# Kernel tuning notes

Hardware: AMD Instinct MI355X
Metric: run time of the kernel (lower is better)

## Reference

```python
import collections
import functools
import itertools
import math
import jax
import jax.numpy as jnp
import numpy as np

# Weight space: RNN-like {W_ih:(784,512), W_hh:(512,512), b:(512,)}, channels last.
N0, N1, C_IN, C_OUT = 784, 512, 16, 16
PERM_SPEC = [[0, 1], [1, 1], [1]]  # perm-group label per dim of each leaf
N_TERMS = [11, 25, 9]  # equivariant basis terms per output leaf (Bell-number products)


def diagonal_slice(X, matching_dims):
    out = jnp.diagonal(X, axis1=matching_dims[0], axis2=matching_dims[1])
    for dim in matching_dims[2:]:
        out = jnp.diagonal(out, axis1=dim, axis2=-1)
    return out


def find_missing_indices(lstA, lstB):
    setB = set(lstB)
    return [i for i, el in enumerate(lstA) if el not in setB]


def get_repeated_idcs(lst):
    index_map = {}
    for index, item in enumerate(lst):
        index_map.setdefault(item, []).append(index)
    return [idcs for idcs in index_map.values() if len(idcs) > 1]


def match_dim_order(X, X_idcs, out_idcs):
    X_idcs_copy = X_idcs[:]
    perm = []
    for idx in out_idcs:
        if idx in X_idcs_copy:
            i = X_idcs_copy.index(idx)
            perm.append(i)
            X_idcs_copy[i] = None
    X = jnp.transpose(X, perm)
    return X, [X_idcs[i] for i in perm]


def remove_idcs(lst, idcs):
    return [l for i, l in enumerate(lst) if i not in idcs]


def move_dims_to_end(X, dims):
    new_in_order = remove_idcs(list(range(X.ndim)), dims) + dims
    return jnp.transpose(X, new_in_order)


def generate_partitions(items):
    if len(items) == 1:
        yield [items]
        return
    first = items[0]
    for subpart in generate_partitions(items[1:]):
        for n, subset in enumerate(subpart):
            yield subpart[:n] + [[first] + subset] + subpart[n + 1:]
        yield [[first]] + subpart


def valid_partitions(indices, perms):
    groups = collections.defaultdict(list)
    for index, perm in zip(indices, perms):
        groups[perm].append(index)
    parts_per_group = [list(generate_partitions(g)) for g in groups.values()]
    for p in itertools.product(*parts_per_group):
        yield [s for s in itertools.chain(*p)]


def gen_terms(out_spec, in_spec, out_shape, inp):
    """Basis terms of an equivariant linear map from in_spec to out_spec."""
    terms = []
    k1, k2 = len(out_spec), len(in_spec)
    for partition in valid_partitions(list(range(k1 + k2)), list(out_spec) + list(in_spec)):
        indices = [-1] * (k1 + k2)
        for subset_idx, subset in enumerate(partition):
            for dim in subset:
                indices[dim] = subset_idx
        out_indices, in_indices = indices[:k1], indices[k1:]
        term = inp
        # Collapse repeated input indices via diagonals.
        while (rep_idcs := get_repeated_idcs(in_indices)):
            term = diagonal_slice(term, rep_idcs[0])
            idx = in_indices[rep_idcs[0][0]]
            in_indices = remove_idcs(in_indices, rep_idcs[0])
            in_indices.append(idx)
        # Mean-reduce input dims that do not appear in the output.
        agg_idcs = find_missing_indices(in_indices, out_indices)
        term = jnp.mean(term, axis=agg_idcs)
        in_indices = remove_idcs(in_indices, agg_idcs)
        # Scatter onto diagonals for repeated output indices.
        for diag_set in get_repeated_idcs(out_indices):
            dim_size, out_idx = out_shape[diag_set[0]], out_indices[diag_set[0]]
            matching_in_dims = [i for i, idx in enumerate(in_indices) if idx == out_idx]
            num_new_dims = len(diag_set) - len(matching_in_dims)
            term = move_dims_to_end(term, matching_in_dims)
            new_term = jnp.zeros(term.shape + (dim_size,) * num_new_dims, dtype=term.dtype)
            diag_slice = (jnp.s_[:],) * (new_term.ndim - len(diag_set)) + (jnp.arange(dim_size),) * len(diag_set)
            if not matching_in_dims:
                term = jnp.expand_dims(term, axis=-1)
            term = new_term.at[diag_slice].add(term)
            in_indices = remove_idcs(in_indices, matching_in_dims)
            in_indices.extend([out_idx] * len(diag_set))
        term, in_indices = match_dim_order(term, in_indices, out_indices)
        term = jnp.expand_dims(term, axis=find_missing_indices(out_indices, in_indices))
        terms.append(term)
    return terms


def setup_inputs() -> dict:
    key = jax.random.key(0)
    ks = jax.random.split(key, 6)
    inp = {
        "w_ih": jax.random.normal(ks[0], (N0, N1, C_IN), jnp.float32),
        "w_hh": jax.random.normal(ks[1], (N1, N1, C_IN), jnp.float32),
        "b": jax.random.normal(ks[2], (N1, C_IN), jnp.float32),
    }
    for i, n in enumerate(N_TERMS):
        scale = math.sqrt(2.0 / (C_IN * n))  # 'he' init, fan_in = c_in * n_terms
        inp[f"theta_{i}"] = scale * jax.random.normal(ks[3 + i], (n, C_IN, C_OUT), jnp.float32)
        inp[f"bias_{i}"] = jnp.zeros((C_OUT,), jnp.float32)
    return inp


def reference(w_ih, w_hh, b, theta_0, theta_1, theta_2, bias_0, bias_1, bias_2):
    flat_params = [w_ih, w_hh, b]
    thetas = [theta_0, theta_1, theta_2]
    biases = [bias_0, bias_1, bias_2]
    outs = []
    for i in range(3):
        terms_i = []
        for j in range(3):
            gen = jax.vmap(
                functools.partial(gen_terms, PERM_SPEC[i], PERM_SPEC[j], flat_params[i].shape),
                in_axes=-1, out_axes=-1)
            terms_i.extend(gen(flat_params[j]))
        out = biases[i]
        for k, term in enumerate(terms_i):
            out = out + term @ thetas[i][k]  # [..., c_in] @ [c_in, c_out]
        outs.append(out)
    return tuple(outs)
```

## Files before the change

### kernel.cpp

```cpp
#include <hip/hip_runtime.h>


#define N0 784
#define N1 512

__global__ __launch_bounds__(256)
void k_stage1(const float* __restrict__ wih, const float* __restrict__ whh,
              float* __restrict__ rm_ih, float* __restrict__ cm_ih,
              float* __restrict__ rm_hh, float* __restrict__ cm_hh,
              float* __restrict__ d_hh) {
  __shared__ float4 red[256];
  int t = threadIdx.x;
  if (blockIdx.x < N0) {
    int a = blockIdx.x;
    const float4* row = (const float4*)(wih + (size_t)a * 8192);
    float4 acc = make_float4(0.f, 0.f, 0.f, 0.f);
    for (int j = t; j < 2048; j += 256) {
      float4 v = row[j];
      acc.x += v.x; acc.y += v.y; acc.z += v.z; acc.w += v.w;
    }
    red[t] = acc; __syncthreads();
    #pragma unroll
    for (int s = 128; s >= 4; s >>= 1) {
      if (t < s) {
        float4 o = red[t + s], m = red[t];
        m.x += o.x; m.y += o.y; m.z += o.z; m.w += o.w;
        red[t] = m;
      }
      __syncthreads();
    }
    if (t < 4) {
      float4 m = red[t];
      const float s = 1.0f / 512.0f;
      float4 o = make_float4(m.x * s, m.y * s, m.z * s, m.w * s);
      ((float4*)(rm_ih + a * 16))[t] = o;
    }
    return;
  }
  int b = blockIdx.x - N0;
  int q = t & 3, g = t >> 2;

  float4 acc = make_float4(0.f, 0.f, 0.f, 0.f);
  for (int a = g; a < N0; a += 64) {
    float4 v = *(const float4*)(wih + (size_t)a * 8192 + b * 16 + q * 4);
    acc.x += v.x; acc.y += v.y; acc.z += v.z; acc.w += v.w;
  }
  red[t] = acc; __syncthreads();
  #pragma unroll
  for (int s = 128; s >= 4; s >>= 1) {
    if (t < s) {
      float4 o = red[t + s], m = red[t];
      m.x += o.x; m.y += o.y; m.z += o.z; m.w += o.w;
      red[t] = m;
    }
    __syncthreads();
  }
  if (t < 4) {
    float4 m = red[t];
    const float s = 1.0f / 784.0f;
    ((float4*)(cm_ih + b * 16))[t] = make_float4(m.x * s, m.y * s, m.z * s, m.w * s);
  }
  __syncthreads();

  const float4* rowp = (const float4*)(whh + (size_t)b * 8192);
  acc = make_float4(0.f, 0.f, 0.f, 0.f);
  for (int n = t; n < 2048; n += 256) {
    float4 v = rowp[n];
    acc.x += v.x; acc.y += v.y; acc.z += v.z; acc.w += v.w;
  }
  red[t] = acc; __syncthreads();
  #pragma unroll
  for (int s = 128; s >= 4; s >>= 1) {
    if (t < s) {
      float4 o = red[t + s], m = red[t];
      m.x += o.x; m.y += o.y; m.z += o.z; m.w += o.w;
      red[t] = m;
    }
    __syncthreads();
  }
  if (t < 4) {
    float4 m = red[t];
    const float s = 1.0f / 512.0f;
    ((float4*)(rm_hh + b * 16))[t] = make_float4(m.x * s, m.y * s, m.z * s, m.w * s);
  }
  __syncthreads();

  acc = make_float4(0.f, 0.f, 0.f, 0.f);
  for (int a = g; a < N1; a += 64) {
    float4 v = *(const float4*)(whh + (size_t)a * 8192 + b * 16 + q * 4);
    acc.x += v.x; acc.y += v.y; acc.z += v.z; acc.w += v.w;
  }
  red[t] = acc; __syncthreads();
  #pragma unroll
  for (int s = 128; s >= 4; s >>= 1) {
    if (t < s) {
      float4 o = red[t + s], m = red[t];
      m.x += o.x; m.y += o.y; m.z += o.z; m.w += o.w;
      red[t] = m;
    }
    __syncthreads();
  }
  if (t < 4) {
    float4 m = red[t];
    const float s = 1.0f / 512.0f;
    ((float4*)(cm_hh + b * 16))[t] = make_float4(m.x * s, m.y * s, m.z * s, m.w * s);
    ((float4*)(d_hh + b * 16))[t] = *(const float4*)(whh + (size_t)b * 8192 + b * 16 + t * 4);
  }
}

__global__ __launch_bounds__(256)
void k_vec(const float* __restrict__ rm_ih, const float* __restrict__ cm_ih,
           const float* __restrict__ rm_hh, const float* __restrict__ cm_hh,
           const float* __restrict__ d_hh, const float* __restrict__ bvec,
           const float* __restrict__ th0, const float* __restrict__ bias0,
           const float* __restrict__ th1, const float* __restrict__ bias1,
           const float* __restrict__ th2, const float* __restrict__ bias2,
           float* __restrict__ A0C, float* __restrict__ B0,
           float* __restrict__ A1C, float* __restrict__ B1,
           float* __restrict__ DD1, float* __restrict__ out2) {
  __shared__ float redf[256];
  __shared__ float4 red4[256];
  __shared__ float gv[4][16];
  __shared__ float sc[64];
  int t = threadIdx.x, ci = t & 15, g = t >> 4;

  {
    float acc = 0.f;
    for (int a = g; a < N0; a += 16) acc += rm_ih[a * 16 + ci];
    redf[t] = acc; __syncthreads();
    for (int s = 128; s >= 16; s >>= 1) { if (t < s) redf[t] += redf[t + s]; __syncthreads(); }
    if (t < 16) gv[0][t] = redf[t] * (1.0f / 784.0f);
    __syncthreads();
    acc = 0.f;
    for (int a = g; a < N1; a += 16) acc += d_hh[a * 16 + ci];
    redf[t] = acc; __syncthreads();
    for (int s = 128; s >= 16; s >>= 1) { if (t < s) redf[t] += redf[t + s]; __syncthreads(); }
    if (t < 16) gv[1][t] = redf[t] * (1.0f / 512.0f);
    __syncthreads();
    acc = 0.f;
    for (int a = g; a < N1; a += 16) acc += rm_hh[a * 16 + ci];
    redf[t] = acc; __syncthreads();
    for (int s = 128; s >= 16; s >>= 1) { if (t < s) redf[t] += redf[t + s]; __syncthreads(); }
    if (t < 16) gv[2][t] = redf[t] * (1.0f / 512.0f);
    __syncthreads();
    acc = 0.f;
    for (int a = g; a < N1; a += 16) acc += bvec[a * 16 + ci];
    redf[t] = acc; __syncthreads();
    for (int s = 128; s >= 16; s >>= 1) { if (t < s) redf[t] += redf[t + s]; __syncthreads(); }
    if (t < 16) gv[3][t] = redf[t] * (1.0f / 512.0f);
    __syncthreads();
  }
  {
    int co = ci, j = g, o = j * 16 + co;
    float g0 = gv[0][j], dm = gv[1][j], gh = gv[2][j], mv = gv[3][j];
    float4 p;
    p.x = g0 * th0[768 + o]  + dm * th0[1280 + o] + gh * th0[2048 + o] + mv * th0[2560 + o];
    p.y = g0 * th1[1024 + o] + dm * th1[2304 + o] + gh * th1[4864 + o] + mv * th1[6144 + o];
    p.z = g0 * th1[512 + o]  + dm * th1[1792 + o] + gh * th1[4096 + o] + mv * th1[5632 + o];
    p.w = g0 * th2[256 + o]  + dm * th2[768 + o]  + gh * th2[1536 + o] + mv * th2[2048 + o];
    red4[t] = p; __syncthreads();
    for (int s = 128; s >= 16; s >>= 1) {
      if (t < s) {
        float4 a = red4[t], b = red4[t + s];
        a.x += b.x; a.y += b.y; a.z += b.z; a.w += b.w;
        red4[t] = a;
      }
      __syncthreads();
    }
    if (t < 16) {
      float4 a = red4[t];
      sc[t] = a.x + bias0[t];
      sc[16 + t] = a.y + bias1[t];
      sc[32 + t] = a.z + bias2[t] * 0.f + 0.f;
      sc[32 + t] = a.z;
      sc[48 + t] = a.w + bias2[t];
    }
    __syncthreads();
  }
  int idx = blockIdx.x * 256 + t;
  int i = idx >> 4, co = idx & 15;
  if (i >= N0) return;
  float a0 = sc[co];
  for (int k = 0; k < 16; k++) a0 += rm_ih[i * 16 + k] * th0[256 + k * 16 + co];
  A0C[idx] = a0;
  if (i < N1) {
    float b0a = 0.f, a1 = sc[16 + co], b1a = 0.f, dd = sc[32 + co], o2 = sc[48 + co];
    for (int k = 0; k < 16; k++) {
      float cmi = cm_ih[i * 16 + k], d = d_hh[i * 16 + k], r = rm_hh[i * 16 + k];
      float cm = cm_hh[i * 16 + k], v = bvec[i * 16 + k];
      int o = k * 16 + co;
      b0a += cmi * th0[512 + o]  + d * th0[1024 + o] + r * th0[1536 + o] + cm * th0[1792 + o] + v * th0[2304 + o];
      a1  += cmi * th1[768 + o]  + d * th1[2048 + o] + r * th1[4352 + o] + cm * th1[4608 + o] + v * th1[5888 + o];
      b1a += cmi * th1[256 + o]  + d * th1[1536 + o] + r * th1[3072 + o] + cm * th1[3840 + o] + v * th1[5376 + o];
      dd  += cmi * th1[0 + o]    + d * th1[1280 + o] + r * th1[2560 + o] + cm * th1[3584 + o] + v * th1[5120 + o];
      o2  += cmi * th2[0 + o]    + d * th2[512 + o]  + r * th2[1024 + o] + cm * th2[1280 + o] + v * th2[1792 + o];
    }
    B0[idx] = b0a; A1C[idx] = a1; B1[idx] = b1a; DD1[idx] = dd; out2[idx] = o2;
  }
}

__global__ __launch_bounds__(256)
void k_out(const float* __restrict__ wih, const float* __restrict__ whh,
           const float* __restrict__ th0, const float* __restrict__ th1,
           const float* __restrict__ A0C, const float* __restrict__ B0,
           const float* __restrict__ A1C, const float* __restrict__ B1,
           const float* __restrict__ DD1,
           float* __restrict__ out0, float* __restrict__ out1) {
  if (blockIdx.x < 1024) {
    int tid = blockIdx.x * 256 + threadIdx.x;
    int q = tid & 3;
    int slot = tid >> 2;
    const int nslots = (1024 * 256) >> 2;
    float4 tq[16];
    #pragma unroll
    for (int k = 0; k < 16; k++) tq[k] = *(const float4*)(th0 + k * 16 + q * 4);
    for (int p = slot; p < N0 * N1; p += nslots) {
      const float4* row = (const float4*)(wih + (size_t)p * 16);
      float4 r0 = row[0], r1 = row[1], r2 = row[2], r3 = row[3];
      int a = p >> 9, bb = p & 511;
      float4 acc = *(const float4*)(A0C + a * 16 + q * 4);
      float4 b4 = *(const float4*)(B0 + bb * 16 + q * 4);
      acc.x += b4.x; acc.y += b4.y; acc.z += b4.z; acc.w += b4.w;
      float wv[16] = { r0.x, r0.y, r0.z, r0.w, r1.x, r1.y, r1.z, r1.w,
                       r2.x, r2.y, r2.z, r2.w, r3.x, r3.y, r3.z, r3.w };
      #pragma unroll
      for (int k = 0; k < 16; k++) {
        acc.x += wv[k] * tq[k].x; acc.y += wv[k] * tq[k].y;
        acc.z += wv[k] * tq[k].z; acc.w += wv[k] * tq[k].w;
      }
      *(float4*)(out0 + (size_t)p * 16 + q * 4) = acc;
    }
  } else {
    int tid = (blockIdx.x - 1024) * 256 + threadIdx.x;
    int q = tid & 7;
    int slot = tid >> 3;
    const int nslots = (1024 * 256) >> 3;
    float2 tA[16], tB[16];
    #pragma unroll
    for (int k = 0; k < 16; k++) {
      tA[k] = *(const float2*)(th1 + 13 * 256 + k * 16 + q * 2);
      tB[k] = *(const float2*)(th1 + 11 * 256 + k * 16 + q * 2);
    }
    for (int p = slot; p < N1 * N1; p += nslots) {
      int a = p >> 9, b = p & 511;
      const float4* ra = (const float4*)(whh + (size_t)p * 16);
      const float4* rt = (const float4*)(whh + (size_t)((b << 9) | a) * 16);
      float4 a0 = ra[0], a1v = ra[1], a2 = ra[2], a3 = ra[3];
      float4 t0 = rt[0], t1v = rt[1], t2 = rt[2], t3 = rt[3];
      float2 acc = *(const float2*)(A1C + a * 16 + q * 2);
      float2 bb = *(const float2*)(B1 + b * 16 + q * 2);
      acc.x += bb.x; acc.y += bb.y;
      if (a == b) {
        float2 dd = *(const float2*)(DD1 + a * 16 + q * 2);
        acc.x += dd.x; acc.y += dd.y;
      }
      float ya[16] = { a0.x, a0.y, a0.z, a0.w, a1v.x, a1v.y, a1v.z, a1v.w,
                       a2.x, a2.y, a2.z, a2.w, a3.x, a3.y, a3.z, a3.w };
      float yt[16] = { t0.x, t0.y, t0.z, t0.w, t1v.x, t1v.y, t1v.z, t1v.w,
                       t2.x, t2.y, t2.z, t2.w, t3.x, t3.y, t3.z, t3.w };
      #pragma unroll
      for (int k = 0; k < 16; k++) {
        acc.x += ya[k] * tA[k].x + yt[k] * tB[k].x;
        acc.y += ya[k] * tA[k].y + yt[k] * tB[k].y;
      }
      *(float2*)(out1 + (size_t)p * 16 + q * 2) = acc;
    }
  }
}

extern "C" void kernel_launch(void* const* d_in, const int* in_sizes, int n_in,
                              void* d_out, int out_size, void* d_ws, size_t ws_size,
                              hipStream_t stream) {
  const float* w_ih = (const float*)d_in[0];
  const float* w_hh = (const float*)d_in[1];
  const float* bvec = (const float*)d_in[2];
  const float *th0, *bias0, *th1, *bias1, *th2, *bias2;
  if (n_in >= 9 && in_sizes[4] == 16) {
    th0 = (const float*)d_in[3]; bias0 = (const float*)d_in[4];
    th1 = (const float*)d_in[5]; bias1 = (const float*)d_in[6];
    th2 = (const float*)d_in[7]; bias2 = (const float*)d_in[8];
  } else {
    th0 = (const float*)d_in[3]; th1 = (const float*)d_in[4]; th2 = (const float*)d_in[5];
    bias0 = (const float*)d_in[6]; bias1 = (const float*)d_in[7]; bias2 = (const float*)d_in[8];
  }
  float* ws    = (float*)d_ws;
  float* rm_ih = ws;
  float* cm_ih = rm_ih + 12544;
  float* rm_hh = cm_ih + 8192;
  float* cm_hh = rm_hh + 8192;
  float* d_hh  = cm_hh + 8192;
  float* A0C   = d_hh + 8192;
  float* B0    = A0C + 12544;
  float* A1C   = B0 + 8192;
  float* B1    = A1C + 8192;
  float* DD1   = B1 + 8192;
  float* out0 = (float*)d_out;
  float* out1 = out0 + (size_t)N0 * N1 * 16;
  float* out2 = out1 + (size_t)N1 * N1 * 16;

  hipLaunchKernelGGL(k_stage1, dim3(N0 + N1), dim3(256), 0, stream,
                     w_ih, w_hh, rm_ih, cm_ih, rm_hh, cm_hh, d_hh);
  hipLaunchKernelGGL(k_vec, dim3(49), dim3(256), 0, stream,
                     rm_ih, cm_ih, rm_hh, cm_hh, d_hh, bvec,
                     th0, bias0, th1, bias1, th2, bias2,
                     A0C, B0, A1C, B1, DD1, out2);
  hipLaunchKernelGGL(k_out, dim3(2048), dim3(256), 0, stream,
                     w_ih, w_hh, th0, th1, A0C, B0, A1C, B1, DD1, out0, out1);
}
```

Baseline: 177.4 us.

## Split stage1 reductions into separate blocks and stage theta in LDS in k_vec

Stage1 now launches one block per reduction (row and column means for both matrices) instead of having each hh block run three reductions one after another. This spreads the serial work across more blocks to raise parallelism. k_vec copies all theta tensors into shared memory, reduces the global vectors with float4 accesses, and uses vectorized per-row loads. The cost is about 46KB of LDS per block and an extra copy of theta in every block. The `i >= N0` guard was removed; this is safe only because 49 blocks exactly covers 784x16 elements.

```diff
diff --git a/kernel.cpp b/kernel.cpp
--- a/kernel.cpp
+++ b/kernel.cpp
@@ -3,6 +3,10 @@
 
 #define N0 784
 #define N1 512
+
+__device__ __forceinline__ float4 f4add(float4 a, float4 b) {
+  a.x += b.x; a.y += b.y; a.z += b.z; a.w += b.w; return a;
+}
 
 __global__ __launch_bounds__(256)
 void k_stage1(const float* __restrict__ wih, const float* __restrict__ whh,
@@ -10,101 +14,40 @@
               float* __restrict__ rm_hh, float* __restrict__ cm_hh,
               float* __restrict__ d_hh) {
   __shared__ float4 red[256];
-  int t = threadIdx.x;
-  if (blockIdx.x < N0) {
-    int a = blockIdx.x;
-    const float4* row = (const float4*)(wih + (size_t)a * 8192);
-    float4 acc = make_float4(0.f, 0.f, 0.f, 0.f);
-    for (int j = t; j < 2048; j += 256) {
-      float4 v = row[j];
-      acc.x += v.x; acc.y += v.y; acc.z += v.z; acc.w += v.w;
-    }
-    red[t] = acc; __syncthreads();
-    #pragma unroll
-    for (int s = 128; s >= 4; s >>= 1) {
-      if (t < s) {
-        float4 o = red[t + s], m = red[t];
-        m.x += o.x; m.y += o.y; m.z += o.z; m.w += o.w;
-        red[t] = m;
-      }
-      __syncthreads();
-    }
-    if (t < 4) {
-      float4 m = red[t];
-      const float s = 1.0f / 512.0f;
-      float4 o = make_float4(m.x * s, m.y * s, m.z * s, m.w * s);
-      ((float4*)(rm_ih + a * 16))[t] = o;
-    }
-    return;
-  }
-  int b = blockIdx.x - N0;
-  int q = t & 3, g = t >> 2;
-
+  int t = threadIdx.x, blk = blockIdx.x;
   float4 acc = make_float4(0.f, 0.f, 0.f, 0.f);
-  for (int a = g; a < N0; a += 64) {
-    float4 v = *(const float4*)(wih + (size_t)a * 8192 + b * 16 + q * 4);
-    acc.x += v.x; acc.y += v.y; acc.z += v.z; acc.w += v.w;
+  float scale;
+  float* dst;
+  if (blk < N0) {
+    const float4* row = (const float4*)(wih + (size_t)blk * 8192);
+    for (int j = t; j < 2048; j += 256) acc = f4add(acc, row[j]);
+    scale = 1.f / 512.f; dst = rm_ih + blk * 16;
+  } else if (blk < N0 + N1) {
+    int b = blk - N0, q = t & 3, g = t >> 2;
+    for (int a = g; a < N0; a += 64)
+      acc = f4add(acc, *(const float4*)(wih + (size_t)a * 8192 + b * 16 + q * 4));
+    scale = 1.f / 784.f; dst = cm_ih + b * 16;
+  } else if (blk < N0 + 2 * N1) {
+    int b = blk - N0 - N1;
+    const float4* row = (const float4*)(whh + (size_t)b * 8192);
+    for (int j = t; j < 2048; j += 256) acc = f4add(acc, row[j]);
+    scale = 1.f / 512.f; dst = rm_hh + b * 16;
+  } else {
+    int b = blk - N0 - 2 * N1, q = t & 3, g = t >> 2;
+    for (int a = g; a < N1; a += 64)
+      acc = f4add(acc, *(const float4*)(whh + (size_t)a * 8192 + b * 16 + q * 4));
+    scale = 1.f / 512.f; dst = cm_hh + b * 16;
+    if (t < 4) ((float4*)(d_hh + b * 16))[t] = *(const float4*)(whh + (size_t)b * 8192 + b * 16 + t * 4);
   }
   red[t] = acc; __syncthreads();
   #pragma unroll
   for (int s = 128; s >= 4; s >>= 1) {
-    if (t < s) {
-      float4 o = red[t + s], m = red[t];
-      m.x += o.x; m.y += o.y; m.z += o.z; m.w += o.w;
-      red[t] = m;
-    }
+    if (t < s) red[t] = f4add(red[t], red[t + s]);
     __syncthreads();
   }
   if (t < 4) {
     float4 m = red[t];
-    const float s = 1.0f / 784.0f;
-    ((float4*)(cm_ih + b * 16))[t] = make_float4(m.x * s, m.y * s, m.z * s, m.w * s);
-  }
-  __syncthreads();
-
-  const float4* rowp = (const float4*)(whh + (size_t)b * 8192);
-  acc = make_float4(0.f, 0.f, 0.f, 0.f);
-  for (int n = t; n < 2048; n += 256) {
-    float4 v = rowp[n];
-    acc.x += v.x; acc.y += v.y; acc.z += v.z; acc.w += v.w;
-  }
-  red[t] = acc; __syncthreads();
-  #pragma unroll
-  for (int s = 128; s >= 4; s >>= 1) {
-    if (t < s) {
-      float4 o = red[t + s], m = red[t];
-      m.x += o.x; m.y += o.y; m.z += o.z; m.w += o.w;
-      red[t] = m;
-    }
-    __syncthreads();
-  }
-  if (t < 4) {
-    float4 m = red[t];
-    const float s = 1.0f / 512.0f;
-    ((float4*)(rm_hh + b * 16))[t] = make_float4(m.x * s, m.y * s, m.z * s, m.w * s);
-  }
-  __syncthreads();
-
-  acc = make_float4(0.f, 0.f, 0.f, 0.f);
-  for (int a = g; a < N1; a += 64) {
-    float4 v = *(const float4*)(whh + (size_t)a * 8192 + b * 16 + q * 4);
-    acc.x += v.x; acc.y += v.y; acc.z += v.z; acc.w += v.w;
-  }
-  red[t] = acc; __syncthreads();
-  #pragma unroll
-  for (int s = 128; s >= 4; s >>= 1) {
-    if (t < s) {
-      float4 o = red[t + s], m = red[t];
-      m.x += o.x; m.y += o.y; m.z += o.z; m.w += o.w;
-      red[t] = m;
-    }
-    __syncthreads();
-  }
-  if (t < 4) {
-    float4 m = red[t];
-    const float s = 1.0f / 512.0f;
-    ((float4*)(cm_hh + b * 16))[t] = make_float4(m.x * s, m.y * s, m.z * s, m.w * s);
-    ((float4*)(d_hh + b * 16))[t] = *(const float4*)(whh + (size_t)b * 8192 + b * 16 + t * 4);
+    ((float4*)dst)[t] = make_float4(m.x * scale, m.y * scale, m.z * scale, m.w * scale);
   }
 }
 
@@ -118,60 +61,64 @@
            float* __restrict__ A0C, float* __restrict__ B0,
            float* __restrict__ A1C, float* __restrict__ B1,
            float* __restrict__ DD1, float* __restrict__ out2) {
-  __shared__ float redf[256];
-  __shared__ float4 red4[256];
+  __shared__ float th[11520];
+  __shared__ float4 red[256];
   __shared__ float gv[4][16];
   __shared__ float sc[64];
-  int t = threadIdx.x, ci = t & 15, g = t >> 4;
-
-  {
-    float acc = 0.f;
-    for (int a = g; a < N0; a += 16) acc += rm_ih[a * 16 + ci];
-    redf[t] = acc; __syncthreads();
-    for (int s = 128; s >= 16; s >>= 1) { if (t < s) redf[t] += redf[t + s]; __syncthreads(); }
-    if (t < 16) gv[0][t] = redf[t] * (1.0f / 784.0f);
-    __syncthreads();
-    acc = 0.f;
-    for (int a = g; a < N1; a += 16) acc += d_hh[a * 16 + ci];
-    redf[t] = acc; __syncthreads();
-    for (int s = 128; s >= 16; s >>= 1) { if (t < s) redf[t] += redf[t + s]; __syncthreads(); }
-    if (t < 16) gv[1][t] = redf[t] * (1.0f / 512.0f);
-    __syncthreads();
-    acc = 0.f;
-    for (int a = g; a < N1; a += 16) acc += rm_hh[a * 16 + ci];
-    redf[t] = acc; __syncthreads();
-    for (int s = 128; s >= 16; s >>= 1) { if (t < s) redf[t] += redf[t + s]; __syncthreads(); }
-    if (t < 16) gv[2][t] = redf[t] * (1.0f / 512.0f);
-    __syncthreads();
-    acc = 0.f;
-    for (int a = g; a < N1; a += 16) acc += bvec[a * 16 + ci];
-    redf[t] = acc; __syncthreads();
-    for (int s = 128; s >= 16; s >>= 1) { if (t < s) redf[t] += redf[t + s]; __syncthreads(); }
-    if (t < 16) gv[3][t] = redf[t] * (1.0f / 512.0f);
-    __syncthreads();
-  }
-  {
-    int co = ci, j = g, o = j * 16 + co;
-    float g0 = gv[0][j], dm = gv[1][j], gh = gv[2][j], mv = gv[3][j];
+  int t = threadIdx.x;
+  {
+    float4* t4 = (float4*)th;
+    const float4* s0 = (const float4*)th0;
+    const float4* s1 = (const float4*)th1;
+    const float4* s2 = (const float4*)th2;
+    for (int j = t; j < 704; j += 256) t4[j] = s0[j];
+    for (int j = t; j < 1600; j += 256) t4[704 + j] = s1[j];
+    for (int j = t; j < 576; j += 256) t4[2304 + j] = s2[j];
+  }
+  int q = t & 3, g = t >> 2;
+  {
+    float4 acc = make_float4(0.f, 0.f, 0.f, 0.f);
+    for (int a = g; a < N0; a += 64) acc = f4add(acc, ((const float4*)rm_ih)[a * 4 + q]);
+    red[t] = acc; __syncthreads();
+    #pragma unroll
+    for (int s = 128; s >= 4; s >>= 1) { if (t < s) red[t] = f4add(red[t], red[t + s]); __syncthreads(); }
+    if (t < 4) {
+      float4 m = red[t];
+      gv[0][t * 4 + 0] = m.x / 784.f; gv[0][t * 4 + 1] = m.y / 784.f;
+      gv[0][t * 4 + 2] = m.z / 784.f; gv[0][t * 4 + 3] = m.w / 784.f;
+    }
+    __syncthreads();
+  }
+  const float* srcs[3] = { d_hh, rm_hh, bvec };
+  #pragma unroll
+  for (int v = 0; v < 3; v++) {
+    float4 acc = make_float4(0.f, 0.f, 0.f, 0.f);
+    for (int a = g; a < N1; a += 64) acc = f4add(acc, ((const float4*)srcs[v])[a * 4 + q]);
+    red[t] = acc; __syncthreads();
+    #pragma unroll
+    for (int s = 128; s >= 4; s >>= 1) { if (t < s) red[t] = f4add(red[t], red[t + s]); __syncthreads(); }
+    if (t < 4) {
+      float4 m = red[t];
+      gv[v + 1][t * 4 + 0] = m.x / 512.f; gv[v + 1][t * 4 + 1] = m.y / 512.f;
+      gv[v + 1][t * 4 + 2] = m.z / 512.f; gv[v + 1][t * 4 + 3] = m.w / 512.f;
+    }
+    __syncthreads();
+  }
+  {
+    int co = t & 15, j = t >> 4, o = j * 16 + co;
+    float g0v = gv[0][j], dm = gv[1][j], gh = gv[2][j], mv = gv[3][j];
     float4 p;
-    p.x = g0 * th0[768 + o]  + dm * th0[1280 + o] + gh * th0[2048 + o] + mv * th0[2560 + o];
-    p.y = g0 * th1[1024 + o] + dm * th1[2304 + o] + gh * th1[4864 + o] + mv * th1[6144 + o];
-    p.z = g0 * th1[512 + o]  + dm * th1[1792 + o] + gh * th1[4096 + o] + mv * th1[5632 + o];
-    p.w = g0 * th2[256 + o]  + dm * th2[768 + o]  + gh * th2[1536 + o] + mv * th2[2048 + o];
-    red4[t] = p; __syncthreads();
-    for (int s = 128; s >= 16; s >>= 1) {
-      if (t < s) {
-        float4 a = red4[t], b = red4[t + s];
-        a.x += b.x; a.y += b.y; a.z += b.z; a.w += b.w;
-        red4[t] = a;
-      }
-      __syncthreads();
-    }
+    p.x = g0v * th[768 + o]         + dm * th[1280 + o]        + gh * th[2048 + o]        + mv * th[2560 + o];
+    p.y = g0v * th[2816 + 1024 + o] + dm * th[2816 + 2304 + o] + gh * th[2816 + 4864 + o] + mv * th[2816 + 6144 + o];
+    p.z = g0v * th[2816 + 512 + o]  + dm * th[2816 + 1792 + o] + gh * th[2816 + 4096 + o] + mv * th[2816 + 5632 + o];
+    p.w = g0v * th[9216 + 256 + o]  + dm * th[9216 + 768 + o]  + gh * th[9216 + 1536 + o] + mv * th[9216 + 2048 + o];
+    red[t] = p; __syncthreads();
+    #pragma unroll
+    for (int s = 128; s >= 16; s >>= 1) { if (t < s) red[t] = f4add(red[t], red[t + s]); __syncthreads(); }
     if (t < 16) {
-      float4 a = red4[t];
+      float4 a = red[t];
       sc[t] = a.x + bias0[t];
       sc[16 + t] = a.y + bias1[t];
-      sc[32 + t] = a.z + bias2[t] * 0.f + 0.f;
       sc[32 + t] = a.z;
       sc[48 + t] = a.w + bias2[t];
     }
@@ -179,21 +126,43 @@
   }
   int idx = blockIdx.x * 256 + t;
   int i = idx >> 4, co = idx & 15;
-  if (i >= N0) return;
   float a0 = sc[co];
-  for (int k = 0; k < 16; k++) a0 += rm_ih[i * 16 + k] * th0[256 + k * 16 + co];
+  {
+    const float4* r4 = (const float4*)(rm_ih + i * 16);
+    #pragma unroll
+    for (int kq = 0; kq < 4; kq++) {
+      float4 r = r4[kq];
+      float vr[4] = { r.x, r.y, r.z, r.w };
+      #pragma unroll
+      for (int e = 0; e < 4; e++) a0 += vr[e] * th[256 + (kq * 4 + e) * 16 + co];
+    }
+  }
   A0C[idx] = a0;
   if (i < N1) {
     float b0a = 0.f, a1 = sc[16 + co], b1a = 0.f, dd = sc[32 + co], o2 = sc[48 + co];
-    for (int k = 0; k < 16; k++) {
-      float cmi = cm_ih[i * 16 + k], d = d_hh[i * 16 + k], r = rm_hh[i * 16 + k];
-      float cm = cm_hh[i * 16 + k], v = bvec[i * 16 + k];
-      int o = k * 16 + co;
-      b0a += cmi * th0[512 + o]  + d * th0[1024 + o] + r * th0[1536 + o] + cm * th0[1792 + o] + v * th0[2304 + o];
-      a1  += cmi * th1[768 + o]  + d * th1[2048 + o] + r * th1[4352 + o] + cm * th1[4608 + o] + v * th1[5888 + o];
-      b1a += cmi * th1[256 + o]  + d * th1[1536 + o] + r * th1[3072 + o] + cm * th1[3840 + o] + v * th1[5376 + o];
-      dd  += cmi * th1[0 + o]    + d * th1[1280 + o] + r * th1[2560 + o] + cm * th1[3584 + o] + v * th1[5120 + o];
-      o2  += cmi * th2[0 + o]    + d * th2[512 + o]  + r * th2[1024 + o] + cm * th2[1280 + o] + v * th2[1792 + o];
+    const float4* c4 = (const float4*)(cm_ih + i * 16);
+    const float4* d4 = (const float4*)(d_hh + i * 16);
+    const float4* r4 = (const float4*)(rm_hh + i * 16);
+    const float4* m4 = (const float4*)(cm_hh + i * 16);
+    const float4* v4 = (const float4*)(bvec + i * 16);
+    #pragma unroll
+    for (int kq = 0; kq < 4; kq++) {
+      float4 cq = c4[kq], dq = d4[kq], rq = r4[kq], mq = m4[kq], vq = v4[kq];
+      float vc[4] = { cq.x, cq.y, cq.z, cq.w };
+      float vd[4] = { dq.x, dq.y, dq.z, dq.w };
+      float vr[4] = { rq.x, rq.y, rq.z, rq.w };
+      float vm[4] = { mq.x, mq.y, mq.z, mq.w };
+      float vb[4] = { vq.x, vq.y, vq.z, vq.w };
+      #pragma unroll
+      for (int e = 0; e < 4; e++) {
+        int o = (kq * 4 + e) * 16 + co;
+        float cmi = vc[e], d = vd[e], r = vr[e], cm = vm[e], v = vb[e];
+        b0a += cmi * th[512 + o]         + d * th[1024 + o]        + r * th[1536 + o]        + cm * th[1792 + o]        + v * th[2304 + o];
+        a1  += cmi * th[2816 + 768 + o]  + d * th[2816 + 2048 + o] + r * th[2816 + 4352 + o] + cm * th[2816 + 4608 + o] + v * th[2816 + 5888 + o];
+        b1a += cmi * th[2816 + 256 + o]  + d * th[2816 + 1536 + o] + r * th[2816 + 3072 + o] + cm * th[2816 + 3840 + o] + v * th[2816 + 5376 + o];
+        dd  += cmi * th[2816 + 0 + o]    + d * th[2816 + 1280 + o] + r * th[2816 + 2560 + o] + cm * th[2816 + 3584 + o] + v * th[2816 + 5120 + o];
+        o2  += cmi * th[9216 + 0 + o]    + d * th[9216 + 512 + o]  + r * th[9216 + 1024 + o] + cm * th[9216 + 1280 + o] + v * th[9216 + 1792 + o];
+      }
     }
     B0[idx] = b0a; A1C[idx] = a1; B1[idx] = b1a; DD1[idx] = dd; out2[idx] = o2;
   }
@@ -298,7 +267,7 @@
   float* out1 = out0 + (size_t)N0 * N1 * 16;
   float* out2 = out1 + (size_t)N1 * N1 * 16;
 
-  hipLaunchKernelGGL(k_stage1, dim3(N0 + N1), dim3(256), 0, stream,
+  hipLaunchKernelGGL(k_stage1, dim3(N0 + 3 * N1), dim3(256), 0, stream,
                      w_ih, w_hh, rm_ih, cm_ih, rm_hh, cm_hh, d_hh);
   hipLaunchKernelGGL(k_vec, dim3(49), dim3(256), 0, stream,
                      rm_ih, cm_ih, rm_hh, cm_hh, d_hh, bvec,
```

New measurement: 153.6 us. 13.4% less time.
